# Kernel tuning notes

Hardware: AMD Instinct MI355X
Metric: run time of the kernel (lower is better)

Reference implementation:

```python
import jax, jax.numpy as jnp
import numpy as np
import itertools

# The repo's eset_ops_4_to_4 builds 69 permutation-equivariant basis ops on a
# rank-4 set tensor x[n, d, i, j, k, l]. We reconstruct the 69-dim basis as all
# order-preserving subset matchings (A, B) with A = kept input index slots,
# B = output slots receiving them (|A| = |B| = s, s = 1..4): sum x over the
# complement of A, then broadcast the reduced tensor into output positions B.
# Count: sum_{s=1..4} C(4,s)^2 = 16 + 36 + 16 + 1 = 69 (Vandermonde C(8,4)=70
# minus the s=0 global-sum term).

def _basis_pairs():
    pairs = []
    for s in range(1, 5):
        for A in itertools.combinations(range(4), s):
            for B in itertools.combinations(range(4), s):
                pairs.append((A, B))
    return pairs  # len == 69

_PAIRS = _basis_pairs()


def _forward(x, coefs, bias):
    # x: (n, d, N, N, N, N); coefs: (d, s_out, 69); bias: (1, s_out, 1,1,1,1)
    out_shape = (x.shape[0], coefs.shape[1]) + x.shape[2:]
    out = jnp.zeros(out_shape, x.dtype)
    for idx, (A, B) in enumerate(_PAIRS):
        sum_axes = tuple(2 + i for i in range(4) if i not in A)
        red = x.sum(axis=sum_axes) if sum_axes else x  # (n, d, N^|A|)
        # mix channels on the SMALL reduced tensor (op and channel mix commute)
        term = jnp.einsum('ds,nd...->ns...', coefs[:, :, idx], red)
        # place kept axes at output slots B (order-preserving), broadcast rest
        for p in range(4):
            if p not in B:
                term = jnp.expand_dims(term, axis=2 + p)
        out = out + term  # broadcasting add == broadcast then accumulate
    return out + bias


def setup_inputs() -> dict:
    key = jax.random.key(0)
    k1, k2 = jax.random.split(key)
    n, d, s_out, N, basis = 2, 8, 8, 32, 69
    x = jax.random.normal(k1, (n, d, N, N, N, N), dtype=jnp.float32)
    std = np.sqrt(2.0 / (d + s_out + basis)).astype(np.float32)
    coefs = std * jax.random.normal(k2, (d, s_out, basis), dtype=jnp.float32)
    bias = jnp.zeros((1, s_out, 1, 1, 1, 1), dtype=jnp.float32)
    return {'x': x, 'coefs': coefs, 'bias': bias}


def reference(x, coefs, bias):
    return _forward(x, coefs, bias)
```

## Files before the change

kernel.cpp:

```cpp
#include <hip/hip_runtime.h>


constexpr size_t R3SZ  = 524288;
constexpr size_t R2SZ  = 16384;
constexpr size_t R1SZ  = 512;
constexpr size_t R3OFF = 0;
constexpr size_t R2OFF = R3OFF + 4 * R3SZ;
constexpr size_t R1OFF = R2OFF + 6 * R2SZ;
constexpr size_t U3OFF = R1OFF + 4 * R1SZ;

__global__ __launch_bounds__(512) void k_red3(const float* __restrict__ x,
                                              float* __restrict__ ws) {
    __shared__ float4 cp[32][4][8];
    __shared__ float  b012[1024];
    __shared__ float4 a2[256];
    const int bid  = blockIdx.x;
    const int t    = threadIdx.x;
    const int half = t >> 8;
    const int tt   = t & 255;
    const int k    = tt >> 3;
    const int l4   = tt & 7;

    if (bid < 512) {
        const int i    = bid & 31;
        const int nd   = bid >> 5;
        const int w4   = (t >> 6) & 3;
        const int lane = t & 63;
        const float* xp = x + ((size_t)nd << 20) + ((size_t)i << 15) + k * 32 + l4 * 4;
        float4 acc = {0.f, 0.f, 0.f, 0.f};
        #pragma unroll
        for (int it = 0; it < 16; ++it) {
            const int j = it * 2 + half;
            float4 v = *(const float4*)(xp + j * 1024);
            acc.x += v.x; acc.y += v.y; acc.z += v.z; acc.w += v.w;
            float h = v.x + v.y + v.z + v.w;
            h += __shfl_xor(h, 1); h += __shfl_xor(h, 2); h += __shfl_xor(h, 4);
            if (l4 == 0) b012[j * 32 + k] = h;
            v.x += __shfl_xor(v.x, 8);  v.y += __shfl_xor(v.y, 8);
            v.z += __shfl_xor(v.z, 8);  v.w += __shfl_xor(v.w, 8);
            v.x += __shfl_xor(v.x, 16); v.y += __shfl_xor(v.y, 16);
            v.z += __shfl_xor(v.z, 16); v.w += __shfl_xor(v.w, 16);
            v.x += __shfl_xor(v.x, 32); v.y += __shfl_xor(v.y, 32);
            v.z += __shfl_xor(v.z, 32); v.w += __shfl_xor(v.w, 32);
            if (lane < 8) cp[j][w4][lane] = v;
        }
        if (half == 1) a2[tt] = acc;
        __syncthreads();
        const size_t base = ((size_t)nd << 15) + ((size_t)i << 10);
        *(float2*)(ws + R3OFF + base + 2 * t) = *(const float2*)(b012 + 2 * t);
        if (half == 0) {
            const int j = tt >> 3, lj = tt & 7;
            float4 s0 = cp[j][0][lj], s1 = cp[j][1][lj];
            float4 s2 = cp[j][2][lj], s3 = cp[j][3][lj];
            float4 s;
            s.x = s0.x + s1.x + s2.x + s3.x;
            s.y = s0.y + s1.y + s2.y + s3.y;
            s.z = s0.z + s1.z + s2.z + s3.z;
            s.w = s0.w + s1.w + s2.w + s3.w;
            *(float4*)(ws + R3OFF + R3SZ + base + j * 32 + lj * 4) = s;
            float4 b = a2[tt];
            a2[tt] = s;
            acc.x += b.x; acc.y += b.y; acc.z += b.z; acc.w += b.w;
            *(float4*)(ws + R3OFF + 2 * R3SZ + base + k * 32 + l4 * 4) = acc;
            float* r23 = ws + R2OFF + 5 * R2SZ + (size_t)nd * 1024 + k * 32 + l4 * 4;
            atomicAdd(r23 + 0, acc.x); atomicAdd(r23 + 1, acc.y);
            atomicAdd(r23 + 2, acc.z); atomicAdd(r23 + 3, acc.w);
        }
        __syncthreads();
        const size_t r2b = (size_t)nd * 1024 + (size_t)i * 32;
        if (t < 32) {
            float s = 0.f;
            #pragma unroll
            for (int kk = 0; kk < 32; ++kk) s += b012[t * 32 + ((kk + t) & 31)];
            ws[R2OFF + 0 * R2SZ + r2b + t] = s;
            float r = s;
            r += __shfl_xor(r, 1);  r += __shfl_xor(r, 2);  r += __shfl_xor(r, 4);
            r += __shfl_xor(r, 8);  r += __shfl_xor(r, 16);
            if (t == 0) ws[R1OFF + 0 * R1SZ + (size_t)nd * 32 + i] = r;
        } else if (t < 64) {
            const int kc = t - 32;
            float s = 0.f;
            #pragma unroll
            for (int j = 0; j < 32; ++j) s += b012[j * 32 + kc];
            ws[R2OFF + 1 * R2SZ + r2b + kc] = s;
            atomicAdd(ws + R1OFF + 2 * R1SZ + (size_t)nd * 32 + kc, s);
        } else if (t < 96) {
            const int l = t - 64;
            const float* af = (const float*)a2;
            float s = 0.f;
            #pragma unroll
            for (int j = 0; j < 32; ++j) s += af[j * 32 + l];
            ws[R2OFF + 2 * R2SZ + r2b + l] = s;
            atomicAdd(ws + R1OFF + 3 * R1SZ + (size_t)nd * 32 + l, s);
        }
    } else {
        const int bb = bid - 512;
        const int j  = bb & 31;
        const int nd = bb >> 5;
        const float* xp = x + ((size_t)nd << 20) + (size_t)j * 1024 + (size_t)tt * 4;
        float4 acc = {0.f, 0.f, 0.f, 0.f};
        #pragma unroll
        for (int it = 0; it < 16; ++it) {
            const int i = it * 2 + half;
            float4 v = *(const float4*)(xp + ((size_t)i << 15));
            acc.x += v.x; acc.y += v.y; acc.z += v.z; acc.w += v.w;
        }
        if (half == 1) a2[tt] = acc;
        __syncthreads();
        const size_t r2b = (size_t)nd * 1024 + (size_t)j * 32;
        if (half == 0) {
            float4 b = a2[tt];
            acc.x += b.x; acc.y += b.y; acc.z += b.z; acc.w += b.w;
            *(float4*)(ws + R3OFF + 3 * R3SZ + ((size_t)nd << 15)
                       + ((size_t)j << 10) + tt * 4) = acc;
            float h = acc.x + acc.y + acc.z + acc.w;
            h += __shfl_xor(h, 1); h += __shfl_xor(h, 2); h += __shfl_xor(h, 4);
            if ((t & 7) == 0) {
                ws[R2OFF + 3 * R2SZ + r2b + k] = h;
                b012[k] = h;
            }
            float4 c2 = acc;
            c2.x += __shfl_xor(c2.x, 8);  c2.y += __shfl_xor(c2.y, 8);
            c2.z += __shfl_xor(c2.z, 8);  c2.w += __shfl_xor(c2.w, 8);
            c2.x += __shfl_xor(c2.x, 16); c2.y += __shfl_xor(c2.y, 16);
            c2.z += __shfl_xor(c2.z, 16); c2.w += __shfl_xor(c2.w, 16);
            c2.x += __shfl_xor(c2.x, 32); c2.y += __shfl_xor(c2.y, 32);
            c2.z += __shfl_xor(c2.z, 32); c2.w += __shfl_xor(c2.w, 32);
            if ((t & 63) < 8) cp[0][t >> 6][t & 63] = c2;
        }
        __syncthreads();
        if (t < 8) {
            float4 s0 = cp[0][0][t], s1 = cp[0][1][t];
            float4 s2 = cp[0][2][t], s3 = cp[0][3][t];
            float4 s;
            s.x = s0.x + s1.x + s2.x + s3.x;
            s.y = s0.y + s1.y + s2.y + s3.y;
            s.z = s0.z + s1.z + s2.z + s3.z;
            s.w = s0.w + s1.w + s2.w + s3.w;
            *(float4*)(ws + R2OFF + 4 * R2SZ + r2b + t * 4) = s;
        }
        if (t < 32) {
            float r = b012[t];
            r += __shfl_xor(r, 1);  r += __shfl_xor(r, 2);  r += __shfl_xor(r, 4);
            r += __shfl_xor(r, 8);  r += __shfl_xor(r, 16);
            if (t == 0) ws[R1OFF + 1 * R1SZ + (size_t)nd * 32 + j] = r;
        }
    }
}

__global__ __launch_bounds__(256) void k_mix3(const float* __restrict__ coefs,
                                              const float* __restrict__ bias,
                                              float* __restrict__ ws) {
    __shared__ float cs[4416];
    for (int idx = threadIdx.x; idx < 4416; idx += 256) cs[idx] = coefs[idx];
    __syncthreads();
    const int blk = blockIdx.x;
    const int cb  = blk & 127;
    const int sop = (blk >> 7) & 3;
    const int n   = blk >> 9;
    const int c   = cb * 256 + threadIdx.x;
    const int p1 = c >> 10, p2 = (c >> 5) & 31, p3 = c & 31;
    const int idxA = p1 * 32 + p2, idxB = p1 * 32 + p3, idxC = p2 * 32 + p3;

    float t2f[2][6] = {};
    #pragma unroll
    for (int a2 = 0; a2 < 6; ++a2) {
        #pragma unroll
        for (int d = 0; d < 8; ++d) {
            const float* base = ws + R2OFF + (size_t)a2 * R2SZ
                                + (size_t)(n * 8 + d) * 1024;
            const float vA = base[idxA], vB = base[idxB], vC = base[idxC];
            #pragma unroll
            for (int so2 = 0; so2 < 2; ++so2) {
                const int cc = (d * 8 + sop * 2 + so2) * 69 + 16 + a2 * 6;
                t2f[so2][0] += cs[cc + 0] * vA;
                t2f[so2][1] += cs[cc + 1] * vB;
                t2f[so2][2] += cs[cc + 3] * vC;
                t2f[so2][3] += cs[cc + 2] * vB;
                t2f[so2][4] += cs[cc + 4] * vC;
                t2f[so2][5] += cs[cc + 5] * vC;
            }
        }
    }
    float t1f[2][4] = {};
    #pragma unroll
    for (int a1 = 0; a1 < 4; ++a1) {
        #pragma unroll
        for (int d = 0; d < 8; ++d) {
            const float* base = ws + R1OFF + (size_t)a1 * R1SZ
                                + (size_t)(n * 8 + d) * 32;
            const float v1 = base[p1], v2 = base[p2], v3 = base[p3];
            #pragma unroll
            for (int so2 = 0; so2 < 2; ++so2) {
                const int cc = (d * 8 + sop * 2 + so2) * 69 + a1 * 4;
                t1f[so2][0] += cs[cc + 0] * v1;
                t1f[so2][1] += cs[cc + 1] * v2;
                t1f[so2][2] += cs[cc + 2] * v3;
                t1f[so2][3] += cs[cc + 3] * v3;
            }
        }
    }

    float v[4][8];
    #pragma unroll
    for (int a = 0; a < 4; ++a)
        #pragma unroll
        for (int d = 0; d < 8; ++d)
            v[a][d] = ws[R3OFF + (size_t)a * R3SZ + (size_t)(n * 8 + d) * 32768 + c];
    #pragma unroll
    for (int b = 0; b < 4; ++b) {
        #pragma unroll
        for (int so2 = 0; so2 < 2; ++so2) {
            const int so = sop * 2 + so2;
            float s = 0.f;
            #pragma unroll
            for (int a = 0; a < 4; ++a)
                #pragma unroll
                for (int d = 0; d < 8; ++d)
                    s += cs[(d * 8 + so) * 69 + 52 + a * 4 + b] * v[a][d];
            if (b == 0) {
                s += t2f[so2][0] + t2f[so2][1] + t2f[so2][2];
                s += t1f[so2][0] + t1f[so2][1] + t1f[so2][2];
                s += bias[so];
            } else if (b == 1) {
                s += t2f[so2][3] + t2f[so2][4] + t1f[so2][3];
            } else if (b == 2) {
                s += t2f[so2][5];
            }
            ws[U3OFF + (size_t)b * R3SZ + (size_t)(n * 8 + so) * 32768 + c] = s;
        }
    }
}

__global__ __launch_bounds__(256) void k_final(const float* __restrict__ x,
                                               const float* __restrict__ coefs,
                                               const float* __restrict__ ws,
                                               float* __restrict__ out) {
    __shared__ float c68[64];
    if (threadIdx.x < 64) c68[threadIdx.x] = coefs[threadIdx.x * 69 + 68];
    __syncthreads();
    const int rb = blockIdx.x;
    const int b  = ((rb & 7) << 8) | (rb >> 3);
    const int j = b & 31;
    const int i = (b >> 5) & 31;
    const int n = b >> 10;
    const int t = threadIdx.x;
    const int k = t >> 3, lq = t & 7;

    float4 xv[8];
    const float* xb = x + ((size_t)n << 23) + ((size_t)i << 15) + j * 1024 + k * 32 + lq * 4;
    #pragma unroll
    for (int d = 0; d < 8; ++d) xv[d] = *(const float4*)(xb + ((size_t)d << 20));

    const float* U = ws + U3OFF;
    const size_t c012 = (size_t)i * 1024 + j * 32 + k;
    const size_t c013 = (size_t)i * 1024 + j * 32 + lq * 4;
    const size_t c023 = (size_t)i * 1024 + k * 32 + lq * 4;
    const size_t c123 = (size_t)j * 1024 + k * 32 + lq * 4;

    #pragma unroll
    for (int so = 0; so < 8; ++so) {
        const size_t nso = (size_t)(n * 8 + so) << 15;
        const float  u0 = U[0 * R3SZ + nso + c012];
        const float4 u1 = *(const float4*)(U + 1 * R3SZ + nso + c013);
        const float4 u2 = *(const float4*)(U + 2 * R3SZ + nso + c023);
        const float4 u3 = *(const float4*)(U + 3 * R3SZ + nso + c123);
        float4 acc;
        acc.x = u0 + u1.x + u2.x + u3.x;
        acc.y = u0 + u1.y + u2.y + u3.y;
        acc.z = u0 + u1.z + u2.z + u3.z;
        acc.w = u0 + u1.w + u2.w + u3.w;
        #pragma unroll
        for (int d = 0; d < 8; ++d) {
            const float w = c68[d * 8 + so];
            acc.x += w * xv[d].x; acc.y += w * xv[d].y;
            acc.z += w * xv[d].z; acc.w += w * xv[d].w;
        }
        *(float4*)(out + ((size_t)(n * 8 + so) << 20) + ((size_t)i << 15)
                   + j * 1024 + k * 32 + lq * 4) = acc;
    }
}

extern "C" void kernel_launch(void* const* d_in, const int* in_sizes, int n_in,
                              void* d_out, int out_size, void* d_ws, size_t ws_size,
                              hipStream_t stream) {
    const float* x     = (const float*)d_in[0];
    const float* coefs = (const float*)d_in[1];
    const float* bias  = (const float*)d_in[2];
    float* out = (float*)d_out;
    float* ws  = (float*)d_ws;

    hipMemsetAsync((void*)(ws + R2OFF + 5 * R2SZ), 0,
                   (R2SZ + 4 * R1SZ) * sizeof(float), stream);
    hipLaunchKernelGGL(k_red3,  dim3(1024), dim3(512), 0, stream, x, ws);
    hipLaunchKernelGGL(k_mix3,  dim3(1024), dim3(256), 0, stream, coefs, bias, ws);
    hipLaunchKernelGGL(k_final, dim3(2048), dim3(256), 0, stream, x, coefs, ws, out);
}
```

Baseline: 213.6 us.

## Restructure mix kernel: one output channel per block, share low-rank terms via LDS

```diff
diff --git a/kernel.cpp b/kernel.cpp
--- a/kernel.cpp
+++ b/kernel.cpp
@@ -148,58 +148,28 @@
     }
 }
 
-__global__ __launch_bounds__(256) void k_mix3(const float* __restrict__ coefs,
+__global__ __launch_bounds__(256) void k_mixF(const float* __restrict__ coefs,
                                               const float* __restrict__ bias,
                                               float* __restrict__ ws) {
-    __shared__ float cs[4416];
-    for (int idx = threadIdx.x; idx < 4416; idx += 256) cs[idx] = coefs[idx];
-    __syncthreads();
+    __shared__ float cs[8][69];
+    __shared__ float tA[8];
+    __shared__ float tB[2][32];
+    __shared__ float t1[4][32];
+    const int tt  = threadIdx.x;
     const int blk = blockIdx.x;
     const int cb  = blk & 127;
-    const int sop = (blk >> 7) & 3;
-    const int n   = blk >> 9;
-    const int c   = cb * 256 + threadIdx.x;
-    const int p1 = c >> 10, p2 = (c >> 5) & 31, p3 = c & 31;
-    const int idxA = p1 * 32 + p2, idxB = p1 * 32 + p3, idxC = p2 * 32 + p3;
-
-    float t2f[2][6] = {};
-    #pragma unroll
-    for (int a2 = 0; a2 < 6; ++a2) {
-        #pragma unroll
-        for (int d = 0; d < 8; ++d) {
-            const float* base = ws + R2OFF + (size_t)a2 * R2SZ
-                                + (size_t)(n * 8 + d) * 1024;
-            const float vA = base[idxA], vB = base[idxB], vC = base[idxC];
-            #pragma unroll
-            for (int so2 = 0; so2 < 2; ++so2) {
-                const int cc = (d * 8 + sop * 2 + so2) * 69 + 16 + a2 * 6;
-                t2f[so2][0] += cs[cc + 0] * vA;
-                t2f[so2][1] += cs[cc + 1] * vB;
-                t2f[so2][2] += cs[cc + 3] * vC;
-                t2f[so2][3] += cs[cc + 2] * vB;
-                t2f[so2][4] += cs[cc + 4] * vC;
-                t2f[so2][5] += cs[cc + 5] * vC;
-            }
-        }
-    }
-    float t1f[2][4] = {};
-    #pragma unroll
-    for (int a1 = 0; a1 < 4; ++a1) {
-        #pragma unroll
-        for (int d = 0; d < 8; ++d) {
-            const float* base = ws + R1OFF + (size_t)a1 * R1SZ
-                                + (size_t)(n * 8 + d) * 32;
-            const float v1 = base[p1], v2 = base[p2], v3 = base[p3];
-            #pragma unroll
-            for (int so2 = 0; so2 < 2; ++so2) {
-                const int cc = (d * 8 + sop * 2 + so2) * 69 + a1 * 4;
-                t1f[so2][0] += cs[cc + 0] * v1;
-                t1f[so2][1] += cs[cc + 1] * v2;
-                t1f[so2][2] += cs[cc + 2] * v3;
-                t1f[so2][3] += cs[cc + 3] * v3;
-            }
-        }
-    }
+    const int so  = (blk >> 7) & 7;
+    const int n   = blk >> 10;
+    const int p1  = cb >> 2;
+    const int p2b = (cb & 3) * 8;
+    const int p2p = tt >> 5, p3 = tt & 31;
+    const int c   = cb * 256 + tt;
+
+    for (int idx = tt; idx < 552; idx += 256) {
+        const int d = idx / 69, r = idx - d * 69;
+        cs[d][r] = coefs[(d * 8 + so) * 69 + r];
+    }
+    const float bso = bias[so];
 
     float v[4][8];
     #pragma unroll
@@ -207,28 +177,108 @@
         #pragma unroll
         for (int d = 0; d < 8; ++d)
             v[a][d] = ws[R3OFF + (size_t)a * R3SZ + (size_t)(n * 8 + d) * 32768 + c];
+    float rv[6][8];
+    {
+        const int pq = (p2b + p2p) * 32 + p3;
+        #pragma unroll
+        for (int a2 = 0; a2 < 6; ++a2)
+            #pragma unroll
+            for (int d = 0; d < 8; ++d)
+                rv[a2][d] = ws[R2OFF + (size_t)a2 * R2SZ
+                               + (size_t)(n * 8 + d) * 1024 + pq];
+    }
+    float rvS[6][8];
+    if (tt < 32) {
+        const int pq = p1 * 32 + tt;
+        #pragma unroll
+        for (int a2 = 0; a2 < 6; ++a2)
+            #pragma unroll
+            for (int d = 0; d < 8; ++d)
+                rvS[a2][d] = ws[R2OFF + (size_t)a2 * R2SZ
+                                + (size_t)(n * 8 + d) * 1024 + pq];
+    } else if (tt < 40) {
+        const int pq = p1 * 32 + p2b + (tt - 32);
+        #pragma unroll
+        for (int a2 = 0; a2 < 6; ++a2)
+            #pragma unroll
+            for (int d = 0; d < 8; ++d)
+                rvS[a2][d] = ws[R2OFF + (size_t)a2 * R2SZ
+                                + (size_t)(n * 8 + d) * 1024 + pq];
+    } else if (tt >= 64 && tt < 96) {
+        const int p = tt - 64;
+        #pragma unroll
+        for (int a1 = 0; a1 < 4; ++a1)
+            #pragma unroll
+            for (int d = 0; d < 8; ++d)
+                rvS[a1][d] = ws[R1OFF + (size_t)a1 * R1SZ
+                                + (size_t)(n * 8 + d) * 32 + p];
+    }
+    __syncthreads();
+
+    float a6[3] = {0.f, 0.f, 0.f};
+    #pragma unroll
+    for (int a2 = 0; a2 < 6; ++a2)
+        #pragma unroll
+        for (int d = 0; d < 8; ++d) {
+            const float* cc = &cs[d][16 + a2 * 6];
+            a6[0] += cc[3] * rv[a2][d];
+            a6[1] += cc[4] * rv[a2][d];
+            a6[2] += cc[5] * rv[a2][d];
+        }
+    if (tt < 32) {
+        float b0 = 0.f, b1v = 0.f;
+        #pragma unroll
+        for (int a2 = 0; a2 < 6; ++a2)
+            #pragma unroll
+            for (int d = 0; d < 8; ++d) {
+                const float* cc = &cs[d][16 + a2 * 6];
+                b0  += cc[1] * rvS[a2][d];
+                b1v += cc[2] * rvS[a2][d];
+            }
+        tB[0][tt] = b0; tB[1][tt] = b1v;
+    } else if (tt < 40) {
+        float a0 = 0.f;
+        #pragma unroll
+        for (int a2 = 0; a2 < 6; ++a2)
+            #pragma unroll
+            for (int d = 0; d < 8; ++d)
+                a0 += cs[d][16 + a2 * 6] * rvS[a2][d];
+        tA[tt - 32] = a0;
+    } else if (tt >= 64 && tt < 96) {
+        const int p = tt - 64;
+        float s0 = 0.f, s1 = 0.f, s2 = 0.f, s3 = 0.f;
+        #pragma unroll
+        for (int a1 = 0; a1 < 4; ++a1)
+            #pragma unroll
+            for (int d = 0; d < 8; ++d) {
+                const float* cc = &cs[d][a1 * 4];
+                s0 += cc[0] * rvS[a1][d];
+                s1 += cc[1] * rvS[a1][d];
+                s2 += cc[2] * rvS[a1][d];
+                s3 += cc[3] * rvS[a1][d];
+            }
+        t1[0][p] = s0; t1[1][p] = s1; t1[2][p] = s2; t1[3][p] = s3;
+    }
+    __syncthreads();
+
     #pragma unroll
     for (int b = 0; b < 4; ++b) {
-        #pragma unroll
-        for (int so2 = 0; so2 < 2; ++so2) {
-            const int so = sop * 2 + so2;
-            float s = 0.f;
-            #pragma unroll
-            for (int a = 0; a < 4; ++a)
-                #pragma unroll
-                for (int d = 0; d < 8; ++d)
-                    s += cs[(d * 8 + so) * 69 + 52 + a * 4 + b] * v[a][d];
-            if (b == 0) {
-                s += t2f[so2][0] + t2f[so2][1] + t2f[so2][2];
-                s += t1f[so2][0] + t1f[so2][1] + t1f[so2][2];
-                s += bias[so];
-            } else if (b == 1) {
-                s += t2f[so2][3] + t2f[so2][4] + t1f[so2][3];
-            } else if (b == 2) {
-                s += t2f[so2][5];
-            }
-            ws[U3OFF + (size_t)b * R3SZ + (size_t)(n * 8 + so) * 32768 + c] = s;
-        }
+        float s = 0.f;
+        #pragma unroll
+        for (int a = 0; a < 4; ++a)
+            #pragma unroll
+            for (int d = 0; d < 8; ++d)
+                s += cs[d][52 + a * 4 + b] * v[a][d];
+        if (b == 0) {
+            s += tA[p2p] + tB[0][p3] + a6[0];
+            s += t1[0][p1] + t1[1][p2b + p2p] + t1[2][p3];
+            s += bso;
+        } else if (b == 1) {
+            s += tB[1][p3] + a6[1] + t1[3][p3];
+        } else if (b == 2) {
+            s += a6[2];
+        }
+        ws[U3OFF + (size_t)b * R3SZ + (size_t)(n * 8 + so) * 32768 + c] = s;
     }
 }
 
@@ -293,6 +343,6 @@
     hipMemsetAsync((void*)(ws + R2OFF + 5 * R2SZ), 0,
                    (R2SZ + 4 * R1SZ) * sizeof(float), stream);
     hipLaunchKernelGGL(k_red3,  dim3(1024), dim3(512), 0, stream, x, ws);
-    hipLaunchKernelGGL(k_mix3,  dim3(1024), dim3(256), 0, stream, coefs, bias, ws);
+    hipLaunchKernelGGL(k_mixF,  dim3(2048), dim3(256), 0, stream, coefs, bias, ws);
     hipLaunchKernelGGL(k_final, dim3(2048), dim3(256), 0, stream, x, coefs, ws, out);
 }
```

Measured after the change: 196.8 us. 7.8% less time.

## Precompute rank-2/rank-1 channel mixes in reduction kernel via last-block counters

Applied to the files above, without the earlier changes.

```diff
diff --git a/kernel.cpp b/kernel.cpp
--- a/kernel.cpp
+++ b/kernel.cpp
@@ -7,13 +7,19 @@
 constexpr size_t R3OFF = 0;
 constexpr size_t R2OFF = R3OFF + 4 * R3SZ;
 constexpr size_t R1OFF = R2OFF + 6 * R2SZ;
-constexpr size_t U3OFF = R1OFF + 4 * R1SZ;
+constexpr size_t T2OFF = R1OFF + 4 * R1SZ;
+constexpr size_t T1OFF = T2OFF + 6 * R2SZ;
+constexpr size_t CTROFF= T1OFF + 4 * R1SZ;
+constexpr size_t U3OFF = CTROFF + 256;
 
 __global__ __launch_bounds__(512) void k_red3(const float* __restrict__ x,
+                                              const float* __restrict__ coefs,
                                               float* __restrict__ ws) {
     __shared__ float4 cp[32][4][8];
     __shared__ float  b012[1024];
     __shared__ float4 a2[256];
+    __shared__ float  c23[8][6][8];
+    __shared__ int    sRow, sN;
     const int bid  = blockIdx.x;
     const int t    = threadIdx.x;
     const int half = t >> 8;
@@ -21,11 +27,13 @@
     const int k    = tt >> 3;
     const int l4   = tt & 7;
 
+    int rowIdx, nIdx, rowP;
     if (bid < 512) {
         const int i    = bid & 31;
         const int nd   = bid >> 5;
         const int w4   = (t >> 6) & 3;
         const int lane = t & 63;
+        rowIdx = (nd >> 3) * 32 + i; nIdx = nd >> 3; rowP = i;
         const float* xp = x + ((size_t)nd << 20) + ((size_t)i << 15) + k * 32 + l4 * 4;
         float4 acc = {0.f, 0.f, 0.f, 0.f};
         #pragma unroll
@@ -97,6 +105,7 @@
         const int bb = bid - 512;
         const int j  = bb & 31;
         const int nd = bb >> 5;
+        rowIdx = 64 + (nd >> 3) * 32 + j; nIdx = nd >> 3; rowP = j;
         const float* xp = x + ((size_t)nd << 20) + (size_t)j * 1024 + (size_t)tt * 4;
         float4 acc = {0.f, 0.f, 0.f, 0.f};
         #pragma unroll
@@ -146,67 +155,95 @@
             if (t == 0) ws[R1OFF + 1 * R1SZ + (size_t)nd * 32 + j] = r;
         }
     }
+
+    __syncthreads();
+    if (t == 0) {
+        __threadfence();
+        int* ctr = (int*)(ws + CTROFF);
+        sRow = (__hip_atomic_fetch_add(&ctr[rowIdx], 1, __ATOMIC_ACQ_REL,
+                                       __HIP_MEMORY_SCOPE_AGENT) == 7);
+        sN   = (__hip_atomic_fetch_add(&ctr[128 + nIdx], 1, __ATOMIC_ACQ_REL,
+                                       __HIP_MEMORY_SCOPE_AGENT) == 511);
+    }
+    __syncthreads();
+    const int n = nIdx;
+    if (sRow) {
+        const int a2lo = (bid < 512) ? 0 : 3;
+        const int a2hi = (bid < 512) ? 3 : 5;
+        for (int id = t; id < 1536; id += 512) {
+            const int b2 = id >> 8, so = (id >> 5) & 7, q = id & 31;
+            float s = 0.f;
+            for (int a = a2lo; a < a2hi; ++a)
+                #pragma unroll
+                for (int d = 0; d < 8; ++d)
+                    s += coefs[(d * 8 + so) * 69 + 16 + a * 6 + b2]
+                         * ws[R2OFF + (size_t)a * R2SZ + (size_t)(n * 8 + d) * 1024
+                              + rowP * 32 + q];
+            atomicAdd(ws + T2OFF + (size_t)b2 * R2SZ + (size_t)(n * 8 + so) * 1024
+                      + rowP * 32 + q, s);
+        }
+    }
+    if (sN) {
+        for (int idx = t; idx < 384; idx += 512) {
+            const int d = idx / 48, rr = idx - d * 48, b2 = rr >> 3, so = rr & 7;
+            c23[d][b2][so] = coefs[(d * 8 + so) * 69 + 46 + b2];
+        }
+        __syncthreads();
+        #pragma unroll
+        for (int m = 0; m < 2; ++m) {
+            const int pq = t + m * 512;
+            float r23[8];
+            #pragma unroll
+            for (int d = 0; d < 8; ++d)
+                r23[d] = ws[R2OFF + 5 * R2SZ + (size_t)(n * 8 + d) * 1024 + pq];
+            #pragma unroll
+            for (int b2 = 0; b2 < 6; ++b2)
+                #pragma unroll
+                for (int so = 0; so < 8; ++so) {
+                    float s = 0.f;
+                    #pragma unroll
+                    for (int d = 0; d < 8; ++d) s += c23[d][b2][so] * r23[d];
+                    atomicAdd(ws + T2OFF + (size_t)b2 * R2SZ
+                              + (size_t)(n * 8 + so) * 1024 + pq, s);
+                }
+        }
+        for (int id = t; id < 1024; id += 512) {
+            const int b1 = id >> 8, so = (id >> 5) & 7, p = id & 31;
+            float s = 0.f;
+            for (int a1 = 0; a1 < 4; ++a1)
+                #pragma unroll
+                for (int d = 0; d < 8; ++d)
+                    s += coefs[(d * 8 + so) * 69 + a1 * 4 + b1]
+                         * ws[R1OFF + (size_t)a1 * R1SZ + (size_t)(n * 8 + d) * 32 + p];
+            ws[T1OFF + (size_t)b1 * R1SZ + (size_t)(n * 8 + so) * 32 + p] = s;
+        }
+    }
 }
 
-__global__ __launch_bounds__(256) void k_mix3(const float* __restrict__ coefs,
-                                              const float* __restrict__ bias,
-                                              float* __restrict__ ws) {
-    __shared__ float cs[4416];
-    for (int idx = threadIdx.x; idx < 4416; idx += 256) cs[idx] = coefs[idx];
-    __syncthreads();
+__global__ __launch_bounds__(256) void k_mix(const float* __restrict__ coefs,
+                                             const float* __restrict__ bias,
+                                             float* __restrict__ ws) {
+    __shared__ float csm[2][8][16];
+    const int tt  = threadIdx.x;
     const int blk = blockIdx.x;
     const int cb  = blk & 127;
     const int sop = (blk >> 7) & 3;
     const int n   = blk >> 9;
-    const int c   = cb * 256 + threadIdx.x;
+    {
+        const int so2 = tt >> 7, d = (tt >> 4) & 7, ab = tt & 15;
+        csm[so2][d][ab] = coefs[(d * 8 + sop * 2 + so2) * 69 + 52 + ab];
+    }
+    const int c  = cb * 256 + tt;
     const int p1 = c >> 10, p2 = (c >> 5) & 31, p3 = c & 31;
-    const int idxA = p1 * 32 + p2, idxB = p1 * 32 + p3, idxC = p2 * 32 + p3;
-
-    float t2f[2][6] = {};
-    #pragma unroll
-    for (int a2 = 0; a2 < 6; ++a2) {
-        #pragma unroll
-        for (int d = 0; d < 8; ++d) {
-            const float* base = ws + R2OFF + (size_t)a2 * R2SZ
-                                + (size_t)(n * 8 + d) * 1024;
-            const float vA = base[idxA], vB = base[idxB], vC = base[idxC];
-            #pragma unroll
-            for (int so2 = 0; so2 < 2; ++so2) {
-                const int cc = (d * 8 + sop * 2 + so2) * 69 + 16 + a2 * 6;
-                t2f[so2][0] += cs[cc + 0] * vA;
-                t2f[so2][1] += cs[cc + 1] * vB;
-                t2f[so2][2] += cs[cc + 3] * vC;
-                t2f[so2][3] += cs[cc + 2] * vB;
-                t2f[so2][4] += cs[cc + 4] * vC;
-                t2f[so2][5] += cs[cc + 5] * vC;
-            }
-        }
-    }
-    float t1f[2][4] = {};
-    #pragma unroll
-    for (int a1 = 0; a1 < 4; ++a1) {
-        #pragma unroll
-        for (int d = 0; d < 8; ++d) {
-            const float* base = ws + R1OFF + (size_t)a1 * R1SZ
-                                + (size_t)(n * 8 + d) * 32;
-            const float v1 = base[p1], v2 = base[p2], v3 = base[p3];
-            #pragma unroll
-            for (int so2 = 0; so2 < 2; ++so2) {
-                const int cc = (d * 8 + sop * 2 + so2) * 69 + a1 * 4;
-                t1f[so2][0] += cs[cc + 0] * v1;
-                t1f[so2][1] += cs[cc + 1] * v2;
-                t1f[so2][2] += cs[cc + 2] * v3;
-                t1f[so2][3] += cs[cc + 3] * v3;
-            }
-        }
-    }
-
     float v[4][8];
     #pragma unroll
     for (int a = 0; a < 4; ++a)
         #pragma unroll
         for (int d = 0; d < 8; ++d)
             v[a][d] = ws[R3OFF + (size_t)a * R3SZ + (size_t)(n * 8 + d) * 32768 + c];
+    __syncthreads();
+    const float* T2 = ws + T2OFF;
+    const float* T1 = ws + T1OFF;
     #pragma unroll
     for (int b = 0; b < 4; ++b) {
         #pragma unroll
@@ -217,17 +254,24 @@
             for (int a = 0; a < 4; ++a)
                 #pragma unroll
                 for (int d = 0; d < 8; ++d)
-                    s += cs[(d * 8 + so) * 69 + 52 + a * 4 + b] * v[a][d];
+                    s += csm[so2][d][a * 4 + b] * v[a][d];
+            const size_t nso = (size_t)(n * 8 + so);
             if (b == 0) {
-                s += t2f[so2][0] + t2f[so2][1] + t2f[so2][2];
-                s += t1f[so2][0] + t1f[so2][1] + t1f[so2][2];
+                s += T2[0 * R2SZ + nso * 1024 + p1 * 32 + p2];
+                s += T2[1 * R2SZ + nso * 1024 + p1 * 32 + p3];
+                s += T2[3 * R2SZ + nso * 1024 + p2 * 32 + p3];
+                s += T1[0 * R1SZ + nso * 32 + p1];
+                s += T1[1 * R1SZ + nso * 32 + p2];
+                s += T1[2 * R1SZ + nso * 32 + p3];
                 s += bias[so];
             } else if (b == 1) {
-                s += t2f[so2][3] + t2f[so2][4] + t1f[so2][3];
+                s += T2[2 * R2SZ + nso * 1024 + p1 * 32 + p3];
+                s += T2[4 * R2SZ + nso * 1024 + p2 * 32 + p3];
+                s += T1[3 * R1SZ + nso * 32 + p3];
             } else if (b == 2) {
-                s += t2f[so2][5];
+                s += T2[5 * R2SZ + nso * 1024 + p2 * 32 + p3];
             }
-            ws[U3OFF + (size_t)b * R3SZ + (size_t)(n * 8 + so) * 32768 + c] = s;
+            ws[U3OFF + (size_t)b * R3SZ + nso * 32768 + c] = s;
         }
     }
 }
@@ -291,8 +335,8 @@
     float* ws  = (float*)d_ws;
 
     hipMemsetAsync((void*)(ws + R2OFF + 5 * R2SZ), 0,
-                   (R2SZ + 4 * R1SZ) * sizeof(float), stream);
-    hipLaunchKernelGGL(k_red3,  dim3(1024), dim3(512), 0, stream, x, ws);
-    hipLaunchKernelGGL(k_mix3,  dim3(1024), dim3(256), 0, stream, coefs, bias, ws);
+                   (U3OFF - (R2OFF + 5 * R2SZ)) * sizeof(float), stream);
+    hipLaunchKernelGGL(k_red3,  dim3(1024), dim3(512), 0, stream, x, coefs, ws);
+    hipLaunchKernelGGL(k_mix,   dim3(1024), dim3(256), 0, stream, coefs, bias, ws);
     hipLaunchKernelGGL(k_final, dim3(2048), dim3(256), 0, stream, x, coefs, ws, out);
 }
```

Result: slower. 405.3 us (+89.7%).
